# Kernel tuning notes

Measured on AMD Instinct MI355X. Metric: run time of the kernel, lower is better.

## Reference

```python
import jax, jax.numpy as jnp
import numpy as np

B, S, F, H, A = 2, 2048, 1024, 16, 64


def setup_inputs() -> dict:
    key = jax.random.key(0)
    ks = jax.random.split(key, 6)
    return {
        "key_input": jax.random.normal(ks[0], (B, S, F), dtype=jnp.float32),
        "query_input": jax.random.normal(ks[1], (B, S, F), dtype=jnp.float32),
        "value_input": jax.random.normal(ks[2], (B, S, F), dtype=jnp.float32),
        "q_w": jax.random.normal(ks[3], (H, F, A), dtype=jnp.float32) * (1.0 / np.sqrt(F)),
        "k_w": jax.random.normal(ks[4], (H, F, A), dtype=jnp.float32) * (1.0 / np.sqrt(F)),
        "v_w": jax.random.normal(ks[5], (H, F, A), dtype=jnp.float32) * (1.0 / np.sqrt(F)),
    }


def reference(key_input, query_input, value_input, q_w, k_w, v_w):
    attention_len = q_w.shape[-1]
    # per-head QKV projections: [B,S,F] x [H,F,A] -> [B,S,H,A]
    keys = jnp.einsum('bsf,hfa->bsha', key_input, k_w)
    queries = jnp.einsum('bsf,hfa->bsha', query_input, q_w)
    values = jnp.einsum('bsf,hfa->bsha', value_input, v_w)
    # scores: [B,H,Q,K]; NOTE: original softmaxes over dim=2 (the query axis)
    energy = jnp.einsum('bqha,bkha->bhqk', queries, keys) / jnp.sqrt(
        jnp.asarray(attention_len, dtype=queries.dtype))
    scores = jax.nn.softmax(energy, axis=2)
    # NOTE: original einsum 'bhqs,bsha->bsha' sums over q, keeps s aligned with values
    return jnp.einsum('bhqs,bsha->bsha', scores, values)
```

## Files before the change

### kernel.cpp

```cpp
#include <hip/hip_runtime.h>
#include <hip/hip_bf16.h>

typedef __bf16 bf16_t;
typedef __bf16 bf16x4 __attribute__((ext_vector_type(4)));
typedef __bf16 bf16x8 __attribute__((ext_vector_type(8)));
typedef float  f32x4  __attribute__((ext_vector_type(4)));

typedef __attribute__((address_space(1))) const void  gvoid_t;
typedef __attribute__((address_space(3))) void        lvoid_t;

static constexpr int Mtot = 4096;
static constexpr int Ntot = 1024;
static constexpr int Ktot = 1024;


__global__ __launch_bounds__(256)
void prepass_kernel(const float* __restrict__ A, const float* __restrict__ W,
                    bf16_t* __restrict__ Ab, bf16_t* __restrict__ Wt)
{
    __shared__ float wtile[64][65];
    const int bid = blockIdx.x, t = threadIdx.x;

    if (bid < 1024) {
        const size_t base = (size_t)bid * 4096 + t * 4;
#pragma unroll
        for (int r = 0; r < 4; ++r) {
            const size_t i = base + (size_t)r * 1024;
            const f32x4 v = *(const f32x4*)(A + i);
            bf16x4 p = {(bf16_t)v[0], (bf16_t)v[1], (bf16_t)v[2], (bf16_t)v[3]};
            *(bf16x4*)(Ab + i) = p;
        }
    } else {
        const int wb = bid - 1024;
        const int head = wb >> 4;
        const int k0 = (wb & 15) * 64;
        const float* wsrc = W + (size_t)head * (Ktot * 64) + (size_t)k0 * 64;
#pragma unroll
        for (int i = 0; i < 4; ++i) {
            const int idx = i * 256 + t;
            const int kr = idx >> 4, a4 = (idx & 15) * 4;
            const f32x4 v = *(const f32x4*)(wsrc + (size_t)kr * 64 + a4);
            wtile[kr][a4 + 0] = v[0]; wtile[kr][a4 + 1] = v[1];
            wtile[kr][a4 + 2] = v[2]; wtile[kr][a4 + 3] = v[3];
        }
        __syncthreads();
#pragma unroll
        for (int i = 0; i < 4; ++i) {
            const int idx = i * 256 + t;
            const int ar = idx >> 4, kc = (idx & 15) * 4;
            bf16x4 p = {(bf16_t)wtile[kc + 0][ar], (bf16_t)wtile[kc + 1][ar],
                        (bf16_t)wtile[kc + 2][ar], (bf16_t)wtile[kc + 3][ar]};
            *(bf16x4*)(Wt + (size_t)(head * 64 + ar) * Ktot + k0 + kc) = p;
        }
    }
}

__global__ __launch_bounds__(256, 2)
void gemm_bf16_kernel(const bf16_t* __restrict__ Ab, const bf16_t* __restrict__ Bt,
                      float* __restrict__ C)
{
    __shared__ bf16_t As[2][64 * 64];
    __shared__ bf16_t Bs[2][128 * 64];

    const int t = threadIdx.x, lane = t & 63, wave = t >> 6;
    const int wm = wave & 1, wn = wave >> 1;

    const int g = (blockIdx.x & 7) * 64 + (blockIdx.x >> 3);
    const int by = g >> 3, bx = g & 7;
    const int bm = by * 64, bn = bx * 128;

    const int lrow = lane & 15;
    const int lkb = (lane >> 4) * 8;

    f32x4 acc[2][4];
#pragma unroll
    for (int mf = 0; mf < 2; ++mf)
#pragma unroll
        for (int nf = 0; nf < 4; ++nf) {
            f32x4 z = {0.f, 0.f, 0.f, 0.f};
            acc[mf][nf] = z;
        }

    auto STAGE = [&](int buf, int k0) {
#pragma unroll
        for (int j = 0; j < 2; ++j) {
            const int chunk = (wave * 2 + j) * 64 + lane;
            const int row = chunk >> 3, kb = (chunk & 7) * 8;
            const bf16_t* gp = Ab + (size_t)(bm + row) * Ktot + k0 + kb;
            __builtin_amdgcn_global_load_lds((gvoid_t*)gp,
                (lvoid_t*)&As[buf][(wave * 2 + j) * 512], 16, 0, 0);
        }
#pragma unroll
        for (int j = 0; j < 4; ++j) {
            const int chunk = (wave * 4 + j) * 64 + lane;
            const int row = chunk >> 3, kb = (chunk & 7) * 8;
            const bf16_t* gp = Bt + (size_t)(bn + row) * Ktot + k0 + kb;
            __builtin_amdgcn_global_load_lds((gvoid_t*)gp,
                (lvoid_t*)&Bs[buf][(wave * 4 + j) * 512], 16, 0, 0);
        }
    };

    STAGE(0, 0);
    __syncthreads();

    constexpr int NT = Ktot / 64;
    for (int tI = 0; tI < NT; ++tI) {
        const int cur = tI & 1;
        if (tI + 1 < NT) STAGE(cur ^ 1, (tI + 1) * 64);

#pragma unroll
        for (int kk = 0; kk < 2; ++kk) {
            bf16x8 af[2], bfr[4];
#pragma unroll
            for (int mf = 0; mf < 2; ++mf)
                af[mf] = *(const bf16x8*)&As[cur][(wm * 32 + mf * 16 + lrow) * 64 + kk * 32 + lkb];
#pragma unroll
            for (int nf = 0; nf < 4; ++nf)
                bfr[nf] = *(const bf16x8*)&Bs[cur][(wn * 64 + nf * 16 + lrow) * 64 + kk * 32 + lkb];
            __builtin_amdgcn_s_setprio(1);
#pragma unroll
            for (int mf = 0; mf < 2; ++mf)
#pragma unroll
                for (int nf = 0; nf < 4; ++nf)
                    acc[mf][nf] = __builtin_amdgcn_mfma_f32_16x16x32_bf16(
                        af[mf], bfr[nf], acc[mf][nf], 0, 0, 0);
            __builtin_amdgcn_s_setprio(0);
        }
        __syncthreads();
    }

#pragma unroll
    for (int mf = 0; mf < 2; ++mf) {
        const int row0 = bm + wm * 32 + mf * 16 + ((lane >> 4) << 2);
#pragma unroll
        for (int nf = 0; nf < 4; ++nf) {
            const int col = bn + wn * 64 + nf * 16 + (lane & 15);
#pragma unroll
            for (int i = 0; i < 4; ++i)
                C[(size_t)(row0 + i) * Ntot + col] = acc[mf][nf][i];
        }
    }
}

static constexpr int FBM = 128, FBN = 128, FBK = 64, FBKP = 72;

__global__ __launch_bounds__(512, 2)
void vproj_fused_kernel(const float* __restrict__ A, const float* __restrict__ W,
                        float* __restrict__ C)
{
    __shared__ bf16_t As[2][FBM][FBKP];
    __shared__ bf16_t Bs[2][FBN][FBKP];

    const int t = threadIdx.x, lane = t & 63, wave = t >> 6;
    const int wm = wave >> 2, wn = wave & 3;
    const int tile = (blockIdx.x & 7) * 32 + (blockIdx.x >> 3);
    const int bm = (tile >> 3) * FBM, bn = (tile & 7) * FBN;

    const int bhead = t >> 8, brem = t & 255;
    const int bkq = brem >> 4, baq = brem & 15;
    const float* const wbase = W + ((size_t)((bn >> 6) + bhead)) * (Ktot * 64)
                                 + (size_t)(bkq * 4) * 64 + baq * 4;
    f32x4 avreg[4], bvreg[4];

    auto load_tile = [&](int k0) {
#pragma unroll
        for (int r = 0; r < 4; ++r) {
            const int idx = r * 512 + t;
            avreg[r] = *(const f32x4*)(A + (size_t)(bm + (idx >> 4)) * Ktot + k0 + (idx & 15) * 4);
        }
        const float* wp = wbase + (size_t)k0 * 64;
#pragma unroll
        for (int r = 0; r < 4; ++r) bvreg[r] = *(const f32x4*)(wp + r * 64);
    };
    auto store_tile = [&](int buf) {
#pragma unroll
        for (int r = 0; r < 4; ++r) {
            const int idx = r * 512 + t;
            bf16x4 p = {(bf16_t)avreg[r][0], (bf16_t)avreg[r][1],
                        (bf16_t)avreg[r][2], (bf16_t)avreg[r][3]};
            *(bf16x4*)&As[buf][idx >> 4][(idx & 15) * 4] = p;
        }
#pragma unroll
        for (int j = 0; j < 4; ++j) {
            bf16x4 p = {(bf16_t)bvreg[0][j], (bf16_t)bvreg[1][j],
                        (bf16_t)bvreg[2][j], (bf16_t)bvreg[3][j]};
            *(bf16x4*)&Bs[buf][bhead * 64 + baq * 4 + j][bkq * 4] = p;
        }
    };

    f32x4 acc[4][2];
#pragma unroll
    for (int mf = 0; mf < 4; ++mf)
#pragma unroll
        for (int nf = 0; nf < 2; ++nf) { f32x4 z = {0,0,0,0}; acc[mf][nf] = z; }

    const int lrow = lane & 15, lkb = (lane >> 4) << 3;
    load_tile(0); store_tile(0); __syncthreads();

    for (int tI = 0; tI < Ktot / FBK; ++tI) {
        const int cur = tI & 1;
        if (tI + 1 < Ktot / FBK) load_tile((tI + 1) * FBK);
#pragma unroll
        for (int kk = 0; kk < 2; ++kk) {
            bf16x8 af[4], bfr[2];
#pragma unroll
            for (int mf = 0; mf < 4; ++mf)
                af[mf] = *(const bf16x8*)&As[cur][wm * 64 + mf * 16 + lrow][kk * 32 + lkb];
#pragma unroll
            for (int nf = 0; nf < 2; ++nf)
                bfr[nf] = *(const bf16x8*)&Bs[cur][wn * 32 + nf * 16 + lrow][kk * 32 + lkb];
#pragma unroll
            for (int mf = 0; mf < 4; ++mf)
#pragma unroll
                for (int nf = 0; nf < 2; ++nf)
                    acc[mf][nf] = __builtin_amdgcn_mfma_f32_16x16x32_bf16(
                        af[mf], bfr[nf], acc[mf][nf], 0, 0, 0);
        }
        if (tI + 1 < Ktot / FBK) store_tile(cur ^ 1);
        __syncthreads();
    }
#pragma unroll
    for (int mf = 0; mf < 4; ++mf) {
        const int row0 = bm + wm * 64 + mf * 16 + ((lane >> 4) << 2);
#pragma unroll
        for (int nf = 0; nf < 2; ++nf) {
            const int col = bn + wn * 32 + nf * 16 + (lane & 15);
#pragma unroll
            for (int i = 0; i < 4; ++i)
                C[(size_t)(row0 + i) * Ntot + col] = acc[mf][nf][i];
        }
    }
}

extern "C" void kernel_launch(void* const* d_in, const int* in_sizes, int n_in,
                              void* d_out, int out_size, void* d_ws, size_t ws_size,
                              hipStream_t stream) {
    (void)in_sizes; (void)n_in; (void)out_size;
    const float* V  = (const float*)d_in[2];
    const float* Vw = (const float*)d_in[5];
    float* out      = (float*)d_out;

    const size_t abBytes = (size_t)Mtot * Ktot * sizeof(bf16_t);
    const size_t wtBytes = (size_t)Ntot * Ktot * sizeof(bf16_t);

    if (ws_size >= abBytes + wtBytes) {
        bf16_t* Ab = (bf16_t*)d_ws;
        bf16_t* Wt = (bf16_t*)((char*)d_ws + abBytes);
        hipLaunchKernelGGL(prepass_kernel, dim3(1024 + 256), dim3(256), 0, stream,
                           V, Vw, Ab, Wt);
        hipLaunchKernelGGL(gemm_bf16_kernel, dim3((Mtot / 64) * (Ntot / 128)),
                           dim3(256), 0, stream, Ab, Wt, out);
    } else {
        hipLaunchKernelGGL(vproj_fused_kernel, dim3(256), dim3(512), 0, stream,
                           V, Vw, out);
    }
}
```

Before: 32.62 us.

## Replace LDS-staged bf16 GEMM with direct global-to-register MFMA operand loads

The bf16 GEMM no longer stages A and B tiles through shared memory with global_load_lds double buffering and per-tile barriers. Each wave now loads its MFMA fragments straight from global memory into registers and computes a 64x32 slice, with the K loop fully unrolled. This removes the LDS traffic and __syncthreads, but every wave re-reads the shared A rows from global/L2, which cuts on-chip reuse, and the uncoalesced 16-byte row-strided loads may expose memory latency.

```diff
diff --git a/kernel.cpp b/kernel.cpp
--- a/kernel.cpp
+++ b/kernel.cpp
@@ -5,9 +5,6 @@
 typedef __bf16 bf16x4 __attribute__((ext_vector_type(4)));
 typedef __bf16 bf16x8 __attribute__((ext_vector_type(8)));
 typedef float  f32x4  __attribute__((ext_vector_type(4)));
-
-typedef __attribute__((address_space(1))) const void  gvoid_t;
-typedef __attribute__((address_space(3))) void        lvoid_t;
 
 static constexpr int Mtot = 4096;
 static constexpr int Ntot = 1024;
@@ -56,85 +53,66 @@
 }
 
 __global__ __launch_bounds__(256, 2)
-void gemm_bf16_kernel(const bf16_t* __restrict__ Ab, const bf16_t* __restrict__ Bt,
-                      float* __restrict__ C)
+void gemm_direct_kernel(const bf16_t* __restrict__ Ab,
+                        const bf16_t* __restrict__ Wt,
+                        float* __restrict__ C)
 {
-    __shared__ bf16_t As[2][64 * 64];
-    __shared__ bf16_t Bs[2][128 * 64];
-
-    const int t = threadIdx.x, lane = t & 63, wave = t >> 6;
-    const int wm = wave & 1, wn = wave >> 1;
-
-    const int g = (blockIdx.x & 7) * 64 + (blockIdx.x >> 3);
+    const int t = threadIdx.x, lane = t & 63, wn = t >> 6;
+
+    const int g  = (blockIdx.x & 7) * 64 + (blockIdx.x >> 3);
     const int by = g >> 3, bx = g & 7;
-    const int bm = by * 64, bn = bx * 128;
-
-    const int lrow = lane & 15;
-    const int lkb = (lane >> 4) * 8;
-
-    f32x4 acc[2][4];
-#pragma unroll
-    for (int mf = 0; mf < 2; ++mf)
-#pragma unroll
-        for (int nf = 0; nf < 4; ++nf) {
+    const int bm = by * 64;
+    const int bn = bx * 128 + wn * 32;
+
+    const int lrow = lane & 15, lq = lane >> 4;
+
+    const bf16_t* ap[4];
+#pragma unroll
+    for (int mf = 0; mf < 4; ++mf)
+        ap[mf] = Ab + (size_t)(bm + mf * 16 + lrow) * Ktot + lq * 8;
+    const bf16_t* bp[2];
+#pragma unroll
+    for (int nf = 0; nf < 2; ++nf)
+        bp[nf] = Wt + (size_t)(bn + nf * 16 + lrow) * Ktot + lq * 8;
+
+    f32x4 acc[4][2];
+#pragma unroll
+    for (int mf = 0; mf < 4; ++mf)
+#pragma unroll
+        for (int nf = 0; nf < 2; ++nf) {
             f32x4 z = {0.f, 0.f, 0.f, 0.f};
             acc[mf][nf] = z;
         }
 
-    auto STAGE = [&](int buf, int k0) {
-#pragma unroll
-        for (int j = 0; j < 2; ++j) {
-            const int chunk = (wave * 2 + j) * 64 + lane;
-            const int row = chunk >> 3, kb = (chunk & 7) * 8;
-            const bf16_t* gp = Ab + (size_t)(bm + row) * Ktot + k0 + kb;
-            __builtin_amdgcn_global_load_lds((gvoid_t*)gp,
-                (lvoid_t*)&As[buf][(wave * 2 + j) * 512], 16, 0, 0);
-        }
-#pragma unroll
-        for (int j = 0; j < 4; ++j) {
-            const int chunk = (wave * 4 + j) * 64 + lane;
-            const int row = chunk >> 3, kb = (chunk & 7) * 8;
-            const bf16_t* gp = Bt + (size_t)(bn + row) * Ktot + k0 + kb;
-            __builtin_amdgcn_global_load_lds((gvoid_t*)gp,
-                (lvoid_t*)&Bs[buf][(wave * 4 + j) * 512], 16, 0, 0);
-        }
-    };
-
-    STAGE(0, 0);
-    __syncthreads();
-
-    constexpr int NT = Ktot / 64;
-    for (int tI = 0; tI < NT; ++tI) {
-        const int cur = tI & 1;
-        if (tI + 1 < NT) STAGE(cur ^ 1, (tI + 1) * 64);
-
+#pragma unroll
+    for (int tI = 0; tI < Ktot / 64; ++tI) {
 #pragma unroll
         for (int kk = 0; kk < 2; ++kk) {
-            bf16x8 af[2], bfr[4];
-#pragma unroll
-            for (int mf = 0; mf < 2; ++mf)
-                af[mf] = *(const bf16x8*)&As[cur][(wm * 32 + mf * 16 + lrow) * 64 + kk * 32 + lkb];
-#pragma unroll
-            for (int nf = 0; nf < 4; ++nf)
-                bfr[nf] = *(const bf16x8*)&Bs[cur][(wn * 64 + nf * 16 + lrow) * 64 + kk * 32 + lkb];
+            const int off = tI * 64 + kk * 32;
+            bf16x8 af[4], bfr[2];
+#pragma unroll
+            for (int mf = 0; mf < 4; ++mf)
+                af[mf] = *(const bf16x8*)(ap[mf] + off);
+#pragma unroll
+            for (int nf = 0; nf < 2; ++nf)
+                bfr[nf] = *(const bf16x8*)(bp[nf] + off);
             __builtin_amdgcn_s_setprio(1);
 #pragma unroll
-            for (int mf = 0; mf < 2; ++mf)
-#pragma unroll
-                for (int nf = 0; nf < 4; ++nf)
+            for (int mf = 0; mf < 4; ++mf)
+#pragma unroll
+                for (int nf = 0; nf < 2; ++nf)
                     acc[mf][nf] = __builtin_amdgcn_mfma_f32_16x16x32_bf16(
                         af[mf], bfr[nf], acc[mf][nf], 0, 0, 0);
             __builtin_amdgcn_s_setprio(0);
         }
-        __syncthreads();
-    }
-
-#pragma unroll
-    for (int mf = 0; mf < 2; ++mf) {
-        const int row0 = bm + wm * 32 + mf * 16 + ((lane >> 4) << 2);
-#pragma unroll
-        for (int nf = 0; nf < 4; ++nf) {
-            const int col = bn + wn * 64 + nf * 16 + (lane & 15);
+    }
+
+#pragma unroll
+    for (int mf = 0; mf < 4; ++mf) {
+        const int row0 = bm + mf * 16 + (lq << 2);
+#pragma unroll
+        for (int nf = 0; nf < 2; ++nf) {
+            const int col = bn + nf * 16 + lrow;
 #pragma unroll
             for (int i = 0; i < 4; ++i)
                 C[(size_t)(row0 + i) * Ntot + col] = acc[mf][nf][i];
@@ -248,8 +226,8 @@
         bf16_t* Wt = (bf16_t*)((char*)d_ws + abBytes);
         hipLaunchKernelGGL(prepass_kernel, dim3(1024 + 256), dim3(256), 0, stream,
                            V, Vw, Ab, Wt);
-        hipLaunchKernelGGL(gemm_bf16_kernel, dim3((Mtot / 64) * (Ntot / 128)),
-                           dim3(256), 0, stream, Ab, Wt, out);
+        hipLaunchKernelGGL(gemm_direct_kernel, dim3(512), dim3(256), 0, stream,
+                           Ab, Wt, out);
     } else {
         hipLaunchKernelGGL(vproj_fused_kernel, dim3(256), dim3(512), 0, stream,
                            V, Vw, out);
```

New measurement: 58.76 us. 1.8x slower.
